# Kernel tuning notes

Hardware: AMD Instinct MI355X
Metric: run time of the kernel (lower is better)

Reference implementation:

```python
import jax, jax.numpy as jnp
import numpy as np
import math

# AAMsoftmax constants (m=0.2, s=30), matching the torch implementation
M = 0.2
S = 30.0
COS_M = math.cos(M)
SIN_M = math.sin(M)
TH = math.cos(math.pi - M)
MM = math.sin(math.pi - M) * M

B, IN, P, C = 4096, 1024, 256, 5994


def _l2norm(v):
    # F.normalize: v / max(||v||, eps)
    n = jnp.sqrt(jnp.sum(v * v, axis=-1, keepdims=True))
    return v / jnp.maximum(n, 1e-12)


def setup_inputs() -> dict:
    key = jax.random.key(0)
    k0, k1, k2, k3 = jax.random.split(key, 4)
    return {
        "x": jax.random.normal(k0, (B, IN), jnp.float32),
        "label": jax.random.randint(k1, (B,), 0, C, dtype=jnp.int32),
        "W_fc": jax.random.normal(k2, (P, IN), jnp.float32) * (1.0 / np.sqrt(IN)),
        "b_fc": jnp.zeros((P,), jnp.float32),
        "W_aam": jax.random.normal(k3, (C, P), jnp.float32) * 0.05,
    }


def reference(x, label, W_fc, b_fc, W_aam):
    # fc layer: [B, IN] -> [B, P]
    e = x @ W_fc.T + b_fc
    # cosine similarity against class prototypes: [B, C]
    cosine = _l2norm(e) @ _l2norm(W_aam).T
    sine = jnp.sqrt(jnp.clip(1.0 - cosine * cosine, 0.0, 1.0))
    phi = cosine * COS_M - sine * SIN_M
    # easy-margin-off fallback: use cosine - mm where angle too large
    phi = jnp.where((cosine - TH) > 0, phi, cosine - MM)
    one_hot = jax.nn.one_hot(label, C, dtype=cosine.dtype)
    logits = (one_hot * phi + (1.0 - one_hot) * cosine) * S
    # cross-entropy (mean over batch)
    logp = jax.nn.log_softmax(logits, axis=-1)
    nll = -jnp.take_along_axis(logp, label[:, None].astype(jnp.int32), axis=1)[:, 0]
    return jnp.mean(nll)
```

## Files before the change

kernel.cpp:

```cpp
#include <hip/hip_runtime.h>
#include <math.h>

typedef __attribute__((ext_vector_type(8))) short bf16x8;
typedef __attribute__((ext_vector_type(4))) float f32x4;

#define AAM_COS_M 0.9800665778412416f
#define AAM_SIN_M 0.19866933079506122f
#define AAM_TH   (-0.9800665778412416f)
#define AAM_MM    0.03973386615901225f
#define C_CLS 5994

__device__ inline ushort f2bf(float f) {
    unsigned x = __float_as_uint(f);
    return (ushort)((x + 0x7fffu + ((x >> 16) & 1u)) >> 16);
}
__device__ inline float bflo(unsigned u) { return __uint_as_float(u << 16); }
__device__ inline float bfhi(unsigned u) { return __uint_as_float(u & 0xffff0000u); }

__global__ __launch_bounds__(256) void to_bf16(const float* __restrict__ s,
                                               ushort* __restrict__ d, int n4) {
    int i = blockIdx.x * 256 + threadIdx.x;
    if (i >= n4) return;
    float4 v = ((const float4*)s)[i];
    ushort4 o;
    o.x = f2bf(v.x); o.y = f2bf(v.y); o.z = f2bf(v.z); o.w = f2bf(v.w);
    ((ushort4*)d)[i] = o;
}

__global__ __launch_bounds__(256) void fc_mfma(const ushort* __restrict__ A,
                                               const ushort* __restrict__ Bm,
                                               const float* __restrict__ bias,
                                               float* __restrict__ C) {
    __shared__ ushort As[128 * 40];
    __shared__ ushort Bs[128 * 40];
    const int tid = threadIdx.x;
    const int lane = tid & 63, w = tid >> 6;
    const int wr = w >> 1, wc = w & 1;
    const int lx = lane & 15, lg = lane >> 4;
    const int rb = blockIdx.x * 128, cb = blockIdx.y * 128;

    f32x4 zero = {0.f, 0.f, 0.f, 0.f};
    f32x4 acc[4][4];
#pragma unroll
    for (int i = 0; i < 4; ++i)
#pragma unroll
        for (int j = 0; j < 4; ++j) acc[i][j] = zero;

    for (int k0 = 0; k0 < 1024; k0 += 32) {
#pragma unroll
        for (int p = 0; p < 2; ++p) {
            int q = tid + p * 256;
            int r = q >> 2, ko = (q & 3) << 3;
            *(float4*)&As[r * 40 + ko] = *(const float4*)&A[(size_t)(rb + r) * 1024 + k0 + ko];
            *(float4*)&Bs[r * 40 + ko] = *(const float4*)&Bm[(size_t)(cb + r) * 1024 + k0 + ko];
        }
        __syncthreads();
        bf16x8 af[4], bfr[4];
#pragma unroll
        for (int f = 0; f < 4; ++f) {
            af[f]  = *(const bf16x8*)&As[(wr * 64 + f * 16 + lx) * 40 + lg * 8];
            bfr[f] = *(const bf16x8*)&Bs[(wc * 64 + f * 16 + lx) * 40 + lg * 8];
        }
#pragma unroll
        for (int i = 0; i < 4; ++i)
#pragma unroll
            for (int j = 0; j < 4; ++j)
                acc[i][j] = __builtin_amdgcn_mfma_f32_16x16x32_bf16(af[i], bfr[j], acc[i][j], 0, 0, 0);
        __syncthreads();
    }
#pragma unroll
    for (int j = 0; j < 4; ++j) {
        int col = cb + wc * 64 + j * 16 + lx;
        float bb = bias[col];
#pragma unroll
        for (int i = 0; i < 4; ++i) {
            int row0 = rb + wr * 64 + i * 16 + lg * 4;
#pragma unroll
            for (int r = 0; r < 4; ++r)
                C[(size_t)(row0 + r) * 256 + col] = acc[i][j][r] + bb;
        }
    }
}

__global__ __launch_bounds__(256) void rownorm_e(const float* __restrict__ E,
                                                 ushort* __restrict__ En) {
    const int wave = threadIdx.x >> 6, lane = threadIdx.x & 63;
    const int row = blockIdx.x * 4 + wave;
    float4 v = ((const float4*)&E[(size_t)row * 256])[lane];
    float ss = v.x * v.x + v.y * v.y + v.z * v.z + v.w * v.w;
#pragma unroll
    for (int m = 32; m >= 1; m >>= 1) ss += __shfl_xor(ss, m, 64);
    float sc = 1.f / fmaxf(sqrtf(ss), 1e-12f);
    ushort4 o;
    o.x = f2bf(v.x * sc); o.y = f2bf(v.y * sc); o.z = f2bf(v.z * sc); o.w = f2bf(v.w * sc);
    ((ushort4*)&En[(size_t)row * 256])[lane] = o;
}

__global__ __launch_bounds__(256) void rownorm_w(const float* __restrict__ W,
                                                 ushort* __restrict__ Wn) {
    const int wave = threadIdx.x >> 6, lane = threadIdx.x & 63;
    const int row = blockIdx.x * 4 + wave;
    if (row >= 6144) return;
    ushort4 o;
    if (row < C_CLS) {
        float4 v = ((const float4*)&W[(size_t)row * 256])[lane];
        float ss = v.x * v.x + v.y * v.y + v.z * v.z + v.w * v.w;
#pragma unroll
        for (int m = 32; m >= 1; m >>= 1) ss += __shfl_xor(ss, m, 64);
        float sc = 1.f / fmaxf(sqrtf(ss), 1e-12f);
        o.x = f2bf(v.x * sc); o.y = f2bf(v.y * sc); o.z = f2bf(v.z * sc); o.w = f2bf(v.w * sc);
    } else {
        o.x = 0; o.y = 0; o.z = 0; o.w = 0;
    }
    ((ushort4*)&Wn[(size_t)row * 256])[lane] = o;
}

__global__ __launch_bounds__(256) void aam_mfma(const ushort* __restrict__ A,
                                                const ushort* __restrict__ Bm,
                                                float* __restrict__ pm,
                                                float* __restrict__ ps) {
    __shared__ ushort As[128 * 40];
    __shared__ ushort Bs[128 * 40];
    const int tid = threadIdx.x;
    const int lane = tid & 63, w = tid >> 6;
    const int wr = w >> 1, wc = w & 1;
    const int lx = lane & 15, lg = lane >> 4;
    const int rb = blockIdx.x * 128;
    const int split = blockIdx.y;

    float mrun[16], srun[16];
#pragma unroll
    for (int idx = 0; idx < 16; ++idx) { mrun[idx] = -INFINITY; srun[idx] = 0.f; }

    f32x4 zero = {0.f, 0.f, 0.f, 0.f};
    for (int t = 0; t < 3; ++t) {
        const int cb = split * 384 + t * 128;
        f32x4 acc[4][4];
#pragma unroll
        for (int i = 0; i < 4; ++i)
#pragma unroll
            for (int j = 0; j < 4; ++j) acc[i][j] = zero;

        for (int k0 = 0; k0 < 256; k0 += 32) {
#pragma unroll
            for (int p = 0; p < 2; ++p) {
                int q = tid + p * 256;
                int r = q >> 2, ko = (q & 3) << 3;
                *(float4*)&As[r * 40 + ko] = *(const float4*)&A[(size_t)(rb + r) * 256 + k0 + ko];
                *(float4*)&Bs[r * 40 + ko] = *(const float4*)&Bm[(size_t)(cb + r) * 256 + k0 + ko];
            }
            __syncthreads();
            bf16x8 af[4], bfr[4];
#pragma unroll
            for (int f = 0; f < 4; ++f) {
                af[f]  = *(const bf16x8*)&As[(wr * 64 + f * 16 + lx) * 40 + lg * 8];
                bfr[f] = *(const bf16x8*)&Bs[(wc * 64 + f * 16 + lx) * 40 + lg * 8];
            }
#pragma unroll
            for (int i = 0; i < 4; ++i)
#pragma unroll
                for (int j = 0; j < 4; ++j)
                    acc[i][j] = __builtin_amdgcn_mfma_f32_16x16x32_bf16(af[i], bfr[j], acc[i][j], 0, 0, 0);
            __syncthreads();
        }

#pragma unroll
        for (int j = 0; j < 4; ++j) {
            int c = cb + wc * 64 + j * 16 + lx;
            if (c < C_CLS) {
#pragma unroll
                for (int i = 0; i < 4; ++i)
#pragma unroll
                    for (int r = 0; r < 4; ++r) {
                        float v = 30.f * acc[i][j][r];
                        int idx = i * 4 + r;
                        float mn = fmaxf(mrun[idx], v);
                        srun[idx] = srun[idx] * __expf(mrun[idx] - mn) + __expf(v - mn);
                        mrun[idx] = mn;
                    }
            }
        }
    }

#pragma unroll
    for (int idx = 0; idx < 16; ++idx) {
#pragma unroll
        for (int msk = 1; msk < 16; msk <<= 1) {
            float om = __shfl_xor(mrun[idx], msk, 64);
            float os = __shfl_xor(srun[idx], msk, 64);
            float mn = fmaxf(mrun[idx], om);
            float sa = (mrun[idx] > -1e37f) ? srun[idx] * __expf(mrun[idx] - mn) : 0.f;
            float sb = (om > -1e37f) ? os * __expf(om - mn) : 0.f;
            mrun[idx] = mn; srun[idx] = sa + sb;
        }
        if (lx == 0) {
            int row = rb + wr * 64 + (idx >> 2) * 16 + lg * 4 + (idx & 3);
            int part = split * 2 + wc;
            pm[part * 4096 + row] = mrun[idx];
            ps[part * 4096 + row] = srun[idx];
        }
    }
}

__global__ __launch_bounds__(256) void cos_label_k(const ushort* __restrict__ En,
                                                   const ushort* __restrict__ Wn,
                                                   const int* __restrict__ lab,
                                                   float* __restrict__ cosl) {
    const int wave = threadIdx.x >> 6, lane = threadIdx.x & 63;
    const int row = blockIdx.x * 4 + wave;
    const int l = lab[row];
    uint2 a = ((const uint2*)&En[(size_t)row * 256])[lane];
    uint2 b = ((const uint2*)&Wn[(size_t)l * 256])[lane];
    float sum = bflo(a.x) * bflo(b.x) + bfhi(a.x) * bfhi(b.x)
              + bflo(a.y) * bflo(b.y) + bfhi(a.y) * bfhi(b.y);
#pragma unroll
    for (int m = 32; m >= 1; m >>= 1) sum += __shfl_xor(sum, m, 64);
    if (lane == 0) cosl[row] = sum;
}

__global__ __launch_bounds__(256) void reduce_nll(const float* __restrict__ pm,
                                                  const float* __restrict__ ps,
                                                  const float* __restrict__ cosl,
                                                  float* __restrict__ out) {
    const int row = blockIdx.x * 256 + threadIdx.x;
    float m = -INFINITY, s = 0.f;
    for (int p = 0; p < 32; ++p) {
        float om = pm[p * 4096 + row];
        float os = ps[p * 4096 + row];
        float mn = fmaxf(m, om);
        float sa = (m > -1e37f) ? s * __expf(m - mn) : 0.f;
        float sb = (om > -1e37f) ? os * __expf(om - mn) : 0.f;
        m = mn; s = sa + sb;
    }
    float cv = cosl[row];
    float sine = sqrtf(fmaxf(1.f - cv * cv, 0.f));
    float phi = cv * AAM_COS_M - sine * AAM_SIN_M;
    phi = ((cv - AAM_TH) > 0.f) ? phi : (cv - AAM_MM);
    float vplain = 30.f * cv, vlab = 30.f * phi;
    float denom = s - __expf(vplain - m) + __expf(vlab - m);
    float nll = m + logf(denom) - vlab;
    float v = nll * (1.f / 4096.f);
#pragma unroll
    for (int msk = 32; msk >= 1; msk >>= 1) v += __shfl_xor(v, msk, 64);
    if ((threadIdx.x & 63) == 0) atomicAdd(out, v);
}

extern "C" void kernel_launch(void* const* d_in, const int* in_sizes, int n_in,
                              void* d_out, int out_size, void* d_ws, size_t ws_size,
                              hipStream_t stream) {
    const float* x    = (const float*)d_in[0];
    const int*   lab  = (const int*)d_in[1];
    const float* Wfc  = (const float*)d_in[2];
    const float* bfc  = (const float*)d_in[3];
    const float* Waam = (const float*)d_in[4];
    float* out = (float*)d_out;

    char* ws = (char*)d_ws;
    ushort* xb   = (ushort*)(ws);
    ushort* Wfcb = (ushort*)(ws + 8388608);
    float*  E    = (float*) (ws + 8912896);
    ushort* En   = (ushort*)(ws);
    ushort* Wn   = (ushort*)(ws + 2097152);
    float*  pm   = (float*) (ws + 13107200);
    float*  ps   = (float*) (ws + 13631488);
    float*  cosl = (float*) (ws + 14155776);

    to_bf16<<<4096, 256, 0, stream>>>(x, xb, 1048576);
    to_bf16<<<256, 256, 0, stream>>>(Wfc, Wfcb, 65536);
    fc_mfma<<<dim3(32, 2), 256, 0, stream>>>(xb, Wfcb, bfc, E);
    rownorm_e<<<1024, 256, 0, stream>>>(E, En);
    rownorm_w<<<1536, 256, 0, stream>>>(Waam, Wn);
    aam_mfma<<<dim3(32, 16), 256, 0, stream>>>(En, Wn, pm, ps);
    cos_label_k<<<1024, 256, 0, stream>>>(En, Wn, lab, cosl);
    hipMemsetAsync(d_out, 0, sizeof(float), stream);
    reduce_nll<<<16, 256, 0, stream>>>(pm, ps, cosl, out);
}
```

Baseline: 145.6 us.

## Use direct global-to-LDS loads, smaller fc tiles, and fuse conversion and reduction kernels

Merges the two bf16 conversion launches into one kernel and fuses the label-cosine and NLL reduction kernels, merging partials with wave shuffles. The fc GEMM drops to 64x64 tiles to launch four times as many blocks. Both GEMMs now stage tiles with global_load_lds instead of register round-trips, using unpadded LDS rows. Risks include LDS bank conflicts from removing padding and more atomic contention, since one atomic is now issued per row.

```diff
diff --git a/kernel.cpp b/kernel.cpp
--- a/kernel.cpp
+++ b/kernel.cpp
@@ -17,10 +17,20 @@
 __device__ inline float bflo(unsigned u) { return __uint_as_float(u << 16); }
 __device__ inline float bfhi(unsigned u) { return __uint_as_float(u & 0xffff0000u); }
 
-__global__ __launch_bounds__(256) void to_bf16(const float* __restrict__ s,
-                                               ushort* __restrict__ d, int n4) {
-    int i = blockIdx.x * 256 + threadIdx.x;
-    if (i >= n4) return;
+__device__ __forceinline__ void gload16(const void* g, void* lds) {
+    __builtin_amdgcn_global_load_lds(
+        (const __attribute__((address_space(1))) unsigned int*)g,
+        (__attribute__((address_space(3))) unsigned int*)lds, 16, 0, 0);
+}
+
+__global__ __launch_bounds__(256) void conv_bf16(const float* __restrict__ x,
+                                                 const float* __restrict__ Wfc,
+                                                 ushort* __restrict__ xb,
+                                                 ushort* __restrict__ wb) {
+    int b = blockIdx.x;
+    const float* s; ushort* d; int i;
+    if (b < 4096) { s = x; d = xb; i = b * 256 + threadIdx.x; }
+    else          { s = Wfc; d = wb; i = (b - 4096) * 256 + threadIdx.x; }
     float4 v = ((const float4*)s)[i];
     ushort4 o;
     o.x = f2bf(v.x); o.y = f2bf(v.y); o.z = f2bf(v.z); o.w = f2bf(v.w);
@@ -31,50 +41,45 @@
                                                const ushort* __restrict__ Bm,
                                                const float* __restrict__ bias,
                                                float* __restrict__ C) {
-    __shared__ ushort As[128 * 40];
-    __shared__ ushort Bs[128 * 40];
-    const int tid = threadIdx.x;
-    const int lane = tid & 63, w = tid >> 6;
+    __shared__ ushort As[64 * 32];
+    __shared__ ushort Bs[64 * 32];
+    const int tid = threadIdx.x, lane = tid & 63, w = tid >> 6;
     const int wr = w >> 1, wc = w & 1;
     const int lx = lane & 15, lg = lane >> 4;
-    const int rb = blockIdx.x * 128, cb = blockIdx.y * 128;
+    const int l4 = lane >> 2, c8 = (lane & 3) << 3;
+    const int rb = blockIdx.x * 64, cb = blockIdx.y * 64;
 
     f32x4 zero = {0.f, 0.f, 0.f, 0.f};
-    f32x4 acc[4][4];
-#pragma unroll
-    for (int i = 0; i < 4; ++i)
-#pragma unroll
-        for (int j = 0; j < 4; ++j) acc[i][j] = zero;
+    f32x4 acc[2][2];
+#pragma unroll
+    for (int i = 0; i < 2; ++i)
+#pragma unroll
+        for (int j = 0; j < 2; ++j) acc[i][j] = zero;
 
     for (int k0 = 0; k0 < 1024; k0 += 32) {
-#pragma unroll
-        for (int p = 0; p < 2; ++p) {
-            int q = tid + p * 256;
-            int r = q >> 2, ko = (q & 3) << 3;
-            *(float4*)&As[r * 40 + ko] = *(const float4*)&A[(size_t)(rb + r) * 1024 + k0 + ko];
-            *(float4*)&Bs[r * 40 + ko] = *(const float4*)&Bm[(size_t)(cb + r) * 1024 + k0 + ko];
-        }
+        gload16(&A[(size_t)(rb + w * 16 + l4) * 1024 + k0 + c8], &As[w * 512]);
+        gload16(&Bm[(size_t)(cb + w * 16 + l4) * 1024 + k0 + c8], &Bs[w * 512]);
         __syncthreads();
-        bf16x8 af[4], bfr[4];
-#pragma unroll
-        for (int f = 0; f < 4; ++f) {
-            af[f]  = *(const bf16x8*)&As[(wr * 64 + f * 16 + lx) * 40 + lg * 8];
-            bfr[f] = *(const bf16x8*)&Bs[(wc * 64 + f * 16 + lx) * 40 + lg * 8];
-        }
-#pragma unroll
-        for (int i = 0; i < 4; ++i)
-#pragma unroll
-            for (int j = 0; j < 4; ++j)
-                acc[i][j] = __builtin_amdgcn_mfma_f32_16x16x32_bf16(af[i], bfr[j], acc[i][j], 0, 0, 0);
+        bf16x8 af[2], bv[2];
+#pragma unroll
+        for (int f = 0; f < 2; ++f) {
+            af[f] = *(const bf16x8*)&As[(wr * 32 + f * 16 + lx) * 32 + lg * 8];
+            bv[f] = *(const bf16x8*)&Bs[(wc * 32 + f * 16 + lx) * 32 + lg * 8];
+        }
+#pragma unroll
+        for (int i = 0; i < 2; ++i)
+#pragma unroll
+            for (int j = 0; j < 2; ++j)
+                acc[i][j] = __builtin_amdgcn_mfma_f32_16x16x32_bf16(af[i], bv[j], acc[i][j], 0, 0, 0);
         __syncthreads();
     }
 #pragma unroll
-    for (int j = 0; j < 4; ++j) {
-        int col = cb + wc * 64 + j * 16 + lx;
+    for (int j = 0; j < 2; ++j) {
+        int col = cb + wc * 32 + j * 16 + lx;
         float bb = bias[col];
 #pragma unroll
-        for (int i = 0; i < 4; ++i) {
-            int row0 = rb + wr * 64 + i * 16 + lg * 4;
+        for (int i = 0; i < 2; ++i) {
+            int row0 = rb + wr * 32 + i * 16 + lg * 4;
 #pragma unroll
             for (int r = 0; r < 4; ++r)
                 C[(size_t)(row0 + r) * 256 + col] = acc[i][j][r] + bb;
@@ -119,12 +124,12 @@
                                                 const ushort* __restrict__ Bm,
                                                 float* __restrict__ pm,
                                                 float* __restrict__ ps) {
-    __shared__ ushort As[128 * 40];
-    __shared__ ushort Bs[128 * 40];
-    const int tid = threadIdx.x;
-    const int lane = tid & 63, w = tid >> 6;
+    __shared__ ushort As[128 * 32];
+    __shared__ ushort Bs[128 * 32];
+    const int tid = threadIdx.x, lane = tid & 63, w = tid >> 6;
     const int wr = w >> 1, wc = w & 1;
     const int lx = lane & 15, lg = lane >> 4;
+    const int l4 = lane >> 2, c8 = (lane & 3) << 3;
     const int rb = blockIdx.x * 128;
     const int split = blockIdx.y;
 
@@ -142,25 +147,22 @@
             for (int j = 0; j < 4; ++j) acc[i][j] = zero;
 
         for (int k0 = 0; k0 < 256; k0 += 32) {
-#pragma unroll
-            for (int p = 0; p < 2; ++p) {
-                int q = tid + p * 256;
-                int r = q >> 2, ko = (q & 3) << 3;
-                *(float4*)&As[r * 40 + ko] = *(const float4*)&A[(size_t)(rb + r) * 256 + k0 + ko];
-                *(float4*)&Bs[r * 40 + ko] = *(const float4*)&Bm[(size_t)(cb + r) * 256 + k0 + ko];
+            gload16(&A[(size_t)(rb + w * 32 + l4) * 256 + k0 + c8], &As[w * 1024]);
+            gload16(&A[(size_t)(rb + w * 32 + 16 + l4) * 256 + k0 + c8], &As[w * 1024 + 512]);
+            gload16(&Bm[(size_t)(cb + w * 32 + l4) * 256 + k0 + c8], &Bs[w * 1024]);
+            gload16(&Bm[(size_t)(cb + w * 32 + 16 + l4) * 256 + k0 + c8], &Bs[w * 1024 + 512]);
+            __syncthreads();
+            bf16x8 af[4], bv[4];
+#pragma unroll
+            for (int f = 0; f < 4; ++f) {
+                af[f] = *(const bf16x8*)&As[(wr * 64 + f * 16 + lx) * 32 + lg * 8];
+                bv[f] = *(const bf16x8*)&Bs[(wc * 64 + f * 16 + lx) * 32 + lg * 8];
             }
-            __syncthreads();
-            bf16x8 af[4], bfr[4];
-#pragma unroll
-            for (int f = 0; f < 4; ++f) {
-                af[f]  = *(const bf16x8*)&As[(wr * 64 + f * 16 + lx) * 40 + lg * 8];
-                bfr[f] = *(const bf16x8*)&Bs[(wc * 64 + f * 16 + lx) * 40 + lg * 8];
-            }
 #pragma unroll
             for (int i = 0; i < 4; ++i)
 #pragma unroll
                 for (int j = 0; j < 4; ++j)
-                    acc[i][j] = __builtin_amdgcn_mfma_f32_16x16x32_bf16(af[i], bfr[j], acc[i][j], 0, 0, 0);
+                    acc[i][j] = __builtin_amdgcn_mfma_f32_16x16x32_bf16(af[i], bv[j], acc[i][j], 0, 0, 0);
             __syncthreads();
         }
 
@@ -202,10 +204,12 @@
     }
 }
 
-__global__ __launch_bounds__(256) void cos_label_k(const ushort* __restrict__ En,
-                                                   const ushort* __restrict__ Wn,
-                                                   const int* __restrict__ lab,
-                                                   float* __restrict__ cosl) {
+__global__ __launch_bounds__(256) void reduce_all(const float* __restrict__ pm,
+                                                  const float* __restrict__ ps,
+                                                  const ushort* __restrict__ En,
+                                                  const ushort* __restrict__ Wn,
+                                                  const int* __restrict__ lab,
+                                                  float* __restrict__ out) {
     const int wave = threadIdx.x >> 6, lane = threadIdx.x & 63;
     const int row = blockIdx.x * 4 + wave;
     const int l = lab[row];
@@ -215,34 +219,29 @@
               + bflo(a.y) * bflo(b.y) + bfhi(a.y) * bfhi(b.y);
 #pragma unroll
     for (int m = 32; m >= 1; m >>= 1) sum += __shfl_xor(sum, m, 64);
-    if (lane == 0) cosl[row] = sum;
-}
-
-__global__ __launch_bounds__(256) void reduce_nll(const float* __restrict__ pm,
-                                                  const float* __restrict__ ps,
-                                                  const float* __restrict__ cosl,
-                                                  float* __restrict__ out) {
-    const int row = blockIdx.x * 256 + threadIdx.x;
-    float m = -INFINITY, s = 0.f;
-    for (int p = 0; p < 32; ++p) {
-        float om = pm[p * 4096 + row];
-        float os = ps[p * 4096 + row];
+    float cv = sum;
+
+    float m, s;
+    if (lane < 32) { m = pm[lane * 4096 + row]; s = ps[lane * 4096 + row]; }
+    else           { m = -INFINITY; s = 0.f; }
+#pragma unroll
+    for (int msk = 1; msk <= 32; msk <<= 1) {
+        float om = __shfl_xor(m, msk, 64);
+        float os = __shfl_xor(s, msk, 64);
         float mn = fmaxf(m, om);
         float sa = (m > -1e37f) ? s * __expf(m - mn) : 0.f;
         float sb = (om > -1e37f) ? os * __expf(om - mn) : 0.f;
         m = mn; s = sa + sb;
     }
-    float cv = cosl[row];
-    float sine = sqrtf(fmaxf(1.f - cv * cv, 0.f));
-    float phi = cv * AAM_COS_M - sine * AAM_SIN_M;
-    phi = ((cv - AAM_TH) > 0.f) ? phi : (cv - AAM_MM);
-    float vplain = 30.f * cv, vlab = 30.f * phi;
-    float denom = s - __expf(vplain - m) + __expf(vlab - m);
-    float nll = m + logf(denom) - vlab;
-    float v = nll * (1.f / 4096.f);
-#pragma unroll
-    for (int msk = 32; msk >= 1; msk >>= 1) v += __shfl_xor(v, msk, 64);
-    if ((threadIdx.x & 63) == 0) atomicAdd(out, v);
+    if (lane == 0) {
+        float sine = sqrtf(fmaxf(1.f - cv * cv, 0.f));
+        float phi = cv * AAM_COS_M - sine * AAM_SIN_M;
+        phi = ((cv - AAM_TH) > 0.f) ? phi : (cv - AAM_MM);
+        float vplain = 30.f * cv, vlab = 30.f * phi;
+        float denom = s - __expf(vplain - m) + __expf(vlab - m);
+        float nll = m + logf(denom) - vlab;
+        atomicAdd(out, nll * (1.f / 4096.f));
+    }
 }
 
 extern "C" void kernel_launch(void* const* d_in, const int* in_sizes, int n_in,
@@ -263,15 +262,12 @@
     ushort* Wn   = (ushort*)(ws + 2097152);
     float*  pm   = (float*) (ws + 13107200);
     float*  ps   = (float*) (ws + 13631488);
-    float*  cosl = (float*) (ws + 14155776);
-
-    to_bf16<<<4096, 256, 0, stream>>>(x, xb, 1048576);
-    to_bf16<<<256, 256, 0, stream>>>(Wfc, Wfcb, 65536);
-    fc_mfma<<<dim3(32, 2), 256, 0, stream>>>(xb, Wfcb, bfc, E);
+
+    conv_bf16<<<4352, 256, 0, stream>>>(x, Wfc, xb, Wfcb);
+    fc_mfma<<<dim3(64, 4), 256, 0, stream>>>(xb, Wfcb, bfc, E);
     rownorm_e<<<1024, 256, 0, stream>>>(E, En);
     rownorm_w<<<1536, 256, 0, stream>>>(Waam, Wn);
     aam_mfma<<<dim3(32, 16), 256, 0, stream>>>(En, Wn, pm, ps);
-    cos_label_k<<<1024, 256, 0, stream>>>(En, Wn, lab, cosl);
     hipMemsetAsync(d_out, 0, sizeof(float), stream);
-    reduce_nll<<<16, 256, 0, stream>>>(pm, ps, cosl, out);
-}
+    reduce_all<<<1024, 256, 0, stream>>>(pm, ps, En, Wn, lab, out);
+}
```

Measured after the change: 178.2 us. +22.4%, slower.
